# Optimization experiments

Hardware: AMD Instinct MI355X
Metric: run time of the kernel (lower is better)

Reference implementation:

```python
import jax, jax.numpy as jnp
import numpy as np

COLUMN_COUNT = 2048
CELLS_PER_COLUMN = 32
NUM_CELLS = COLUMN_COUNT * CELLS_PER_COLUMN
MAX_SEGMENTS = 16
MAX_SYNAPSES = 32
ACTIVATION_THRESHOLD = 13
PERMANENCE_CONNECTED = 0.5


def setup_inputs() -> dict:
    key = jax.random.key(0)
    k1, k2, k3, k4, k5 = jax.random.split(key, 5)
    active_columns = jax.random.randint(k1, (COLUMN_COUNT,), 0, 2).astype(jnp.float32)
    prev_active = jax.random.randint(k2, (NUM_CELLS,), 0, 2).astype(jnp.float32)
    prev_predictive = jax.random.randint(k3, (NUM_CELLS,), 0, 2).astype(jnp.float32)
    seg_pre = jax.random.randint(k4, (NUM_CELLS, MAX_SEGMENTS, MAX_SYNAPSES), 0, NUM_CELLS, dtype=jnp.int32)
    seg_perm = jax.random.uniform(k5, (NUM_CELLS, MAX_SEGMENTS, MAX_SYNAPSES), dtype=jnp.float32)
    return {
        'active_columns': active_columns,
        'prev_active': prev_active,
        'prev_predictive': prev_predictive,
        'seg_pre': seg_pre,
        'seg_perm': seg_perm,
    }


def _best_segment_activity(seg_pre, connected, active_vec):
    """Per cell: max over segments of (# synapses that are connected AND whose
    presynaptic cell is active). Mirrors _get_segment_activity/_get_best_matching_segment."""
    pre_active = active_vec[seg_pre] > 0          # [N, S, K] irregular gather
    counts = jnp.sum(connected & pre_active, axis=-1)  # [N, S]
    return jnp.max(counts, axis=-1)               # [N]


def reference(active_columns, prev_active, prev_predictive, seg_pre, seg_perm):
    C, cpc = COLUMN_COUNT, CELLS_PER_COLUMN
    connected = seg_perm >= PERMANENCE_CONNECTED   # [N, S, K]

    col_active = active_columns > 0                           # [C]
    pred = (prev_predictive > 0).reshape(C, cpc)              # [C, cpc]
    col_has_pred = jnp.any(pred, axis=1)                      # [C]

    # Active cells: predicted cells if any prediction in column, else burst (all cells).
    new_active = jnp.where(col_active[:, None],
                           jnp.where(col_has_pred[:, None], pred, True),
                           False)                             # [C, cpc]
    active_flat = new_active.reshape(-1).astype(jnp.float32)  # [N]

    # New predictive cells: any segment with activity >= activation_threshold
    # w.r.t. the NEW active set.
    best_act = _best_segment_activity(seg_pre, connected, active_flat)  # [N]
    new_predictive = (best_act >= ACTIVATION_THRESHOLD).astype(jnp.float32)

    # Anomaly: fraction of active columns with no predicted cell.
    n_active_cols = jnp.sum(col_active)
    n_predicted = jnp.sum(col_active & col_has_pred)
    anomaly = (1.0 - n_predicted / jnp.maximum(n_active_cols, 1)).astype(jnp.float32)

    return active_flat, new_predictive, anomaly


if __name__ == '__main__':
    out = reference(**setup_inputs())
    print([o.shape for o in out])
```

## Files before the change

kernel.cpp:

```cpp
#include <hip/hip_runtime.h>

#define COLS    2048
#define CPC     32
#define NCELLS  65536
#define SEGS    16
#define SYN     32
#define THRESH  13

#define CPB     8
#define PREDICT_GRID (NCELLS / CPB)

__global__ __launch_bounds__(256) void tm_active_kernel(
    const float* __restrict__ active_columns,
    const float* __restrict__ prev_predictive,
    float* __restrict__ out_active,
    unsigned int* __restrict__ ws_mask,
    unsigned char* __restrict__ ws_flags)
{
    int n = blockIdx.x * 256 + threadIdx.x;
    int c = n >> 5;
    int j = n & 31;
    int lane = threadIdx.x & 63;

    bool predbit    = prev_predictive[n] > 0.0f;
    bool col_active = active_columns[c] > 0.0f;

    unsigned long long pb = __ballot(predbit);
    unsigned int colmask = (lane < 32) ? (unsigned int)pb : (unsigned int)(pb >> 32);
    bool has_pred = (colmask != 0u);

    bool active = col_active && (has_pred ? predbit : true);
    out_active[n] = active ? 1.0f : 0.0f;

    unsigned long long ab = __ballot(active);
    if (lane == 0)  ws_mask[c] = (unsigned int)ab;
    if (lane == 32) ws_mask[c] = (unsigned int)(ab >> 32);

    if (j == 0)
        ws_flags[c] = (unsigned char)((col_active ? 1 : 0) |
                                      ((col_active && has_pred) ? 2 : 0));
}

typedef const __attribute__((address_space(1))) void* gas_ptr;
typedef __attribute__((address_space(3)))       void* las_ptr;

__device__ __forceinline__ void dma_1kb(const char* g, char* lds, int lane) {
    __builtin_amdgcn_global_load_lds((gas_ptr)(g + lane * 16), (las_ptr)lds, 16, 0, 0);
}

__global__ __launch_bounds__(256) void tm_predict_kernel(
    const int*   __restrict__ seg_pre,
    const float* __restrict__ seg_perm,
    const unsigned int* __restrict__ ws_mask,
    const unsigned char* __restrict__ ws_flags,
    float* __restrict__ out_pred,
    float* __restrict__ out_anomaly)
{
    __shared__ unsigned int mask[COLS];
    __shared__ char pre_lds [CPB * 2048];
    __shared__ char perm_lds[CPB * 2048];

    int tid  = threadIdx.x;
    int wave = tid >> 6;
    int lane = tid & 63;
    int cell0 = blockIdx.x * CPB;

    #pragma unroll
    for (int k = 0; k < 2; ++k) {
        int c = 2 * wave + k;
        const char* gp = (const char*)(seg_pre  + (size_t)(cell0 + c) * 512);
        const char* gq = (const char*)(seg_perm + (size_t)(cell0 + c) * 512);
        dma_1kb(gp,        pre_lds  + c * 2048,        lane);
        dma_1kb(gp + 1024, pre_lds  + c * 2048 + 1024, lane);
        dma_1kb(gq,        perm_lds + c * 2048,        lane);
        dma_1kb(gq + 1024, perm_lds + c * 2048 + 1024, lane);
    }

    #pragma unroll
    for (int i = 0; i < 2; ++i)
        ((uint4*)mask)[tid + 256 * i] = ((const uint4*)ws_mask)[tid + 256 * i];

    __syncthreads();

    #pragma unroll
    for (int k = 0; k < 2; ++k) {
        int c = 2 * wave + k;
        const int4*   pl = (const int4*)  (pre_lds  + c * 2048);
        const float4* ql = (const float4*)(perm_lds + c * 2048);

        int4   p0 = pl[lane], p1 = pl[lane + 64];
        float4 q0 = ql[lane], q1 = ql[lane + 64];

        int c0 = 0, c1 = 0;
        c0 += (q0.x >= 0.5f && ((mask[(unsigned)p0.x >> 5] >> ((unsigned)p0.x & 31u)) & 1u)) ? 1 : 0;
        c0 += (q0.y >= 0.5f && ((mask[(unsigned)p0.y >> 5] >> ((unsigned)p0.y & 31u)) & 1u)) ? 1 : 0;
        c0 += (q0.z >= 0.5f && ((mask[(unsigned)p0.z >> 5] >> ((unsigned)p0.z & 31u)) & 1u)) ? 1 : 0;
        c0 += (q0.w >= 0.5f && ((mask[(unsigned)p0.w >> 5] >> ((unsigned)p0.w & 31u)) & 1u)) ? 1 : 0;
        c1 += (q1.x >= 0.5f && ((mask[(unsigned)p1.x >> 5] >> ((unsigned)p1.x & 31u)) & 1u)) ? 1 : 0;
        c1 += (q1.y >= 0.5f && ((mask[(unsigned)p1.y >> 5] >> ((unsigned)p1.y & 31u)) & 1u)) ? 1 : 0;
        c1 += (q1.z >= 0.5f && ((mask[(unsigned)p1.z >> 5] >> ((unsigned)p1.z & 31u)) & 1u)) ? 1 : 0;
        c1 += (q1.w >= 0.5f && ((mask[(unsigned)p1.w >> 5] >> ((unsigned)p1.w & 31u)) & 1u)) ? 1 : 0;

        int v = c0 | (c1 << 16);
        v += __shfl_xor(v, 1, 64);
        v += __shfl_xor(v, 2, 64);
        v += __shfl_xor(v, 4, 64);
        int m = max(v & 0xffff, v >> 16);
        m = max(m, __shfl_xor(m, 8, 64));
        m = max(m, __shfl_xor(m, 16, 64));
        m = max(m, __shfl_xor(m, 32, 64));

        if (lane == 0)
            out_pred[cell0 + c] = (m >= THRESH) ? 1.0f : 0.0f;
    }

    if (blockIdx.x == 0 && tid < 64) {
        const unsigned int* f = (const unsigned int*)ws_flags;
        int na = 0, np = 0;
        #pragma unroll
        for (int i = 0; i < 8; ++i) {
            unsigned w = f[tid * 8 + i];
            na += __popc(w & 0x01010101u);
            np += __popc(w & 0x02020202u);
        }
        int v = na | (np << 16);
        v += __shfl_xor(v, 1, 64);
        v += __shfl_xor(v, 2, 64);
        v += __shfl_xor(v, 4, 64);
        v += __shfl_xor(v, 8, 64);
        v += __shfl_xor(v, 16, 64);
        v += __shfl_xor(v, 32, 64);
        if (tid == 0) {
            int NA = v & 0xffff, NP = v >> 16;
            *out_anomaly = 1.0f - (float)NP / (float)(NA > 1 ? NA : 1);
        }
    }
}

extern "C" void kernel_launch(void* const* d_in, const int* in_sizes, int n_in,
                              void* d_out, int out_size, void* d_ws, size_t ws_size,
                              hipStream_t stream) {
    const float* active_columns  = (const float*)d_in[0];
    const float* prev_predictive = (const float*)d_in[2];
    const int*   seg_pre         = (const int*)d_in[3];
    const float* seg_perm        = (const float*)d_in[4];
    float* out = (float*)d_out;

    unsigned int*  ws_mask  = (unsigned int*)d_ws;
    unsigned char* ws_flags = (unsigned char*)d_ws + COLS * sizeof(unsigned int);

    tm_active_kernel<<<NCELLS / 256, 256, 0, stream>>>(
        active_columns, prev_predictive, out, ws_mask, ws_flags);

    tm_predict_kernel<<<PREDICT_GRID, 256, 0, stream>>>(
        seg_pre, seg_perm, ws_mask, ws_flags,
        out + NCELLS, out + 2 * NCELLS);
}
```

Measured before the change: 281.2 us.

## Double-buffer per-wave segment DMA across 16 cells per wave in predict kernel

The predict kernel drops from 8192 blocks of 8 cells to 1024 blocks, and each wave now processes 16 consecutive cells. Each wave prefetches the next cell's seg_pre and seg_perm rows into an alternate LDS buffer with global_load_lds, then waits on vmcnt before computing on the current buffer. This overlaps DMA with the gather and count work. It also loads the 8 KB active-cell mask into LDS only once per 64 cells instead of once per 8. The trade-off is only one cell's load in flight per wave, and fewer blocks to hide latency.

```diff
diff --git a/kernel.cpp b/kernel.cpp
--- a/kernel.cpp
+++ b/kernel.cpp
@@ -7,8 +7,8 @@
 #define SYN     32
 #define THRESH  13
 
-#define CPB     8
-#define PREDICT_GRID (NCELLS / CPB)
+#define PRED_BLOCKS      1024
+#define CELLS_PER_WAVE   16
 
 __global__ __launch_bounds__(256) void tm_active_kernel(
     const float* __restrict__ active_columns,
@@ -48,6 +48,9 @@
     __builtin_amdgcn_global_load_lds((gas_ptr)(g + lane * 16), (las_ptr)lds, 16, 0, 0);
 }
 
+#define WAITCNT_VM4 0x0F74
+#define WAITCNT_VM0 0x0F70
+
 __global__ __launch_bounds__(256) void tm_predict_kernel(
     const int*   __restrict__ seg_pre,
     const float* __restrict__ seg_perm,
@@ -57,36 +60,48 @@
     float* __restrict__ out_anomaly)
 {
     __shared__ unsigned int mask[COLS];
-    __shared__ char pre_lds [CPB * 2048];
-    __shared__ char perm_lds[CPB * 2048];
+    __shared__ char bufs[4 * 2 * 4096];
 
     int tid  = threadIdx.x;
     int wave = tid >> 6;
     int lane = tid & 63;
-    int cell0 = blockIdx.x * CPB;
-
-    #pragma unroll
-    for (int k = 0; k < 2; ++k) {
-        int c = 2 * wave + k;
-        const char* gp = (const char*)(seg_pre  + (size_t)(cell0 + c) * 512);
-        const char* gq = (const char*)(seg_perm + (size_t)(cell0 + c) * 512);
-        dma_1kb(gp,        pre_lds  + c * 2048,        lane);
-        dma_1kb(gp + 1024, pre_lds  + c * 2048 + 1024, lane);
-        dma_1kb(gq,        perm_lds + c * 2048,        lane);
-        dma_1kb(gq + 1024, perm_lds + c * 2048 + 1024, lane);
-    }
 
     #pragma unroll
     for (int i = 0; i < 2; ++i)
         ((uint4*)mask)[tid + 256 * i] = ((const uint4*)ws_mask)[tid + 256 * i];
-
     __syncthreads();
 
+    int base = (blockIdx.x * 4 + wave) * CELLS_PER_WAVE;
+    char* mybuf = bufs + wave * 2 * 4096;
+
+    {
+        const char* gp = (const char*)(seg_pre  + (size_t)base * 512);
+        const char* gq = (const char*)(seg_perm + (size_t)base * 512);
+        dma_1kb(gp,        mybuf,        lane);
+        dma_1kb(gp + 1024, mybuf + 1024, lane);
+        dma_1kb(gq,        mybuf + 2048, lane);
+        dma_1kb(gq + 1024, mybuf + 3072, lane);
+    }
+
     #pragma unroll
-    for (int k = 0; k < 2; ++k) {
-        int c = 2 * wave + k;
-        const int4*   pl = (const int4*)  (pre_lds  + c * 2048);
-        const float4* ql = (const float4*)(perm_lds + c * 2048);
+    for (int i = 0; i < CELLS_PER_WAVE; ++i) {
+        if (i + 1 < CELLS_PER_WAVE) {
+            char* nb = mybuf + ((i + 1) & 1) * 4096;
+            const char* gp = (const char*)(seg_pre  + (size_t)(base + i + 1) * 512);
+            const char* gq = (const char*)(seg_perm + (size_t)(base + i + 1) * 512);
+            dma_1kb(gp,        nb,        lane);
+            dma_1kb(gp + 1024, nb + 1024, lane);
+            dma_1kb(gq,        nb + 2048, lane);
+            dma_1kb(gq + 1024, nb + 3072, lane);
+        }
+        __builtin_amdgcn_sched_barrier(0);
+        if (i + 1 < CELLS_PER_WAVE) __builtin_amdgcn_s_waitcnt(WAITCNT_VM4);
+        else                        __builtin_amdgcn_s_waitcnt(WAITCNT_VM0);
+        __builtin_amdgcn_sched_barrier(0);
+
+        char* sb = mybuf + (i & 1) * 4096;
+        const int4*   pl = (const int4*)  sb;
+        const float4* ql = (const float4*)(sb + 2048);
 
         int4   p0 = pl[lane], p1 = pl[lane + 64];
         float4 q0 = ql[lane], q1 = ql[lane + 64];
@@ -111,7 +126,7 @@
         m = max(m, __shfl_xor(m, 32, 64));
 
         if (lane == 0)
-            out_pred[cell0 + c] = (m >= THRESH) ? 1.0f : 0.0f;
+            out_pred[base + i] = (m >= THRESH) ? 1.0f : 0.0f;
     }
 
     if (blockIdx.x == 0 && tid < 64) {
@@ -152,7 +167,7 @@
     tm_active_kernel<<<NCELLS / 256, 256, 0, stream>>>(
         active_columns, prev_predictive, out, ws_mask, ws_flags);
 
-    tm_predict_kernel<<<PREDICT_GRID, 256, 0, stream>>>(
+    tm_predict_kernel<<<PRED_BLOCKS, 256, 0, stream>>>(
         seg_pre, seg_perm, ws_mask, ws_flags,
         out + NCELLS, out + 2 * NCELLS);
 }
```

Measured after the change: 288.2 us. 1.02x slower.
